# Kernel optimization log

Measured on AMD Instinct MI355X. Metric: run time of the kernel, lower is better.

The kernel has to match this reference:

```python
import jax, jax.numpy as jnp
import numpy as np

C_IN, C_INT = 256, 128


def setup_inputs() -> dict:
    key = jax.random.key(0)
    ks = jax.random.split(key, 7)
    B, H, W = 8, 64, 64
    s_in = 1.0 / np.sqrt(C_IN)
    return {
        "x": jax.random.normal(ks[0], (B, C_IN, H, W), dtype=jnp.float32),
        "w_theta": jax.random.uniform(ks[1], (C_INT, C_IN), jnp.float32, -s_in, s_in),
        "b_theta": jax.random.uniform(ks[2], (C_INT,), jnp.float32, -s_in, s_in),
        "w_phi": jax.random.uniform(ks[3], (C_INT, C_IN), jnp.float32, -s_in, s_in),
        "b_phi": jax.random.uniform(ks[4], (C_INT,), jnp.float32, -s_in, s_in),
        "w_g": jax.random.uniform(ks[5], (C_INT, C_IN), jnp.float32, -s_in, s_in),
        "b_g": jax.random.uniform(ks[6], (C_INT,), jnp.float32, -s_in, s_in),
    }


def reference(x, w_theta, b_theta, w_phi, b_phi, w_g, b_g):
    B, C, H, W = x.shape
    # flatten spatial: [B, N, C], 1x1 conv == per-position linear
    xf = x.reshape(B, C, H * W).transpose(0, 2, 1)  # [B, N, C_in]
    theta = jnp.einsum('bnc,dc->bnd', xf, w_theta) + b_theta  # [B, N, C_int]
    phi = jnp.einsum('bnc,dc->bnd', xf, w_phi) + b_phi        # [B, N, C_int]
    g = jnp.einsum('bnc,dc->bnd', xf, w_g) + b_g              # [B, N, C_int]
    f = jnp.einsum('bnd,bmd->bnm', theta, phi)  # [B, N, N] unscaled scores
    f_div_C = jax.nn.softmax(f, axis=-1)
    y = jnp.einsum('bnm,bmd->bnd', f_div_C, g)  # [B, N, C_int]
    # back to [B, C_int, H, W]
    return y.transpose(0, 2, 1).reshape(B, C_INT, H, W)
```

## Files before the change

### kernel.cpp

```cpp
#include <hip/hip_runtime.h>

typedef __attribute__((ext_vector_type(8))) short bf8;
typedef __attribute__((ext_vector_type(4))) float f4;
typedef unsigned short u16;

constexpr int B_ = 8, CIN = 256, CINT = 128, NN = 4096;
constexpr float L2E = 1.44269504088896f;

__device__ __forceinline__ u16 f2bf(float f) {
  unsigned int u = __builtin_bit_cast(unsigned int, f);
  u += 0x7FFFu + ((u >> 16) & 1u);
  return (u16)(u >> 16);
}

__device__ __forceinline__ void glds16(const void* g, void* l) {
  __builtin_amdgcn_global_load_lds(
      (const __attribute__((address_space(1))) unsigned int*)g,
      (__attribute__((address_space(3))) unsigned int*)l, 16, 0, 0);
}

__global__ __launch_bounds__(256) void prep_kernel(
    const float* __restrict__ wth, const float* __restrict__ wph,
    const float* __restrict__ wg, u16* __restrict__ wbf)
{
  int i = blockIdx.x * 256 + threadIdx.x;
  const float* src = (i < 32768) ? wth : (i < 65536) ? wph : wg;
  wbf[i] = f2bf(src[i & 32767]);
}

__global__ __launch_bounds__(256) void proj_kernel(
    const float* __restrict__ x, const u16* __restrict__ wbf,
    const float* __restrict__ bth, const float* __restrict__ bph,
    const float* __restrict__ bg,
    u16* __restrict__ theta, u16* __restrict__ phiT, u16* __restrict__ gTt)
{
  const int b = blockIdx.y, n0 = blockIdx.x * 64;
  const int tid = threadIdx.x, w = tid >> 6, l = tid & 63;
  const int lr = l & 15, lg = l >> 4;
  __shared__ __align__(16) u16 sx[64 * 256];

  const float* xb = x + (size_t)b * CIN * NN + n0;
  #pragma unroll
  for (int pass = 0; pass < 8; ++pass) {
    const int cb = w * 8 + pass * 32;
    u16 tmp[8];
    #pragma unroll
    for (int i = 0; i < 8; ++i) tmp[i] = f2bf(xb[(size_t)(cb + i) * NN + l]);
    uint4 v;
    v.x = (unsigned)tmp[0] | ((unsigned)tmp[1] << 16);
    v.y = (unsigned)tmp[2] | ((unsigned)tmp[3] << 16);
    v.z = (unsigned)tmp[4] | ((unsigned)tmp[5] << 16);
    v.w = (unsigned)tmp[6] | ((unsigned)tmp[7] << 16);
    *(uint4*)&sx[l * 256 + (((w + pass * 4) ^ (l & 7)) << 3)] = v;
  }
  __syncthreads();

  #pragma unroll
  for (int dti = 0; dti < 6; ++dti) {
    const int dt = w * 6 + dti;
    const int mat = dt >> 3, d0 = (dt & 7) * 16;
    const float* Bv = (mat == 0) ? bth : (mat == 1) ? bph : bg;
    const u16* wrow = wbf + mat * 32768 + (size_t)(d0 + lr) * 256 + lg * 8;
    bf8 wf[8];
    #pragma unroll
    for (int ks = 0; ks < 8; ++ks) wf[ks] = *(const bf8*)(wrow + ks * 32);

    #pragma unroll
    for (int mt = 0; mt < 4; ++mt) {
      f4 acc = {0.f, 0.f, 0.f, 0.f};
      const int row = mt * 16 + lr;
      #pragma unroll
      for (int ks = 0; ks < 8; ++ks) {
        bf8 bx = *(const bf8*)&sx[row * 256 + (((ks * 4 + lg) ^ (lr & 7)) << 3)];
        acc = __builtin_amdgcn_mfma_f32_16x16x32_bf16(wf[ks], bx, acc, 0, 0, 0);
      }
      const int m = n0 + mt * 16 + lr;
      const int dlo = d0 + lg * 4;
      if (mat == 0) {
        ushort4 h4;
        h4.x = f2bf(acc[0] + Bv[dlo + 0]);
        h4.y = f2bf(acc[1] + Bv[dlo + 1]);
        h4.z = f2bf(acc[2] + Bv[dlo + 2]);
        h4.w = f2bf(acc[3] + Bv[dlo + 3]);
        *(ushort4*)&theta[((size_t)b * NN + m) * CINT + dlo] = h4;
      } else if (mat == 1) {
        const int kt = m >> 5, r32 = m & 31;
        ushort4 h4;
        h4.x = f2bf((acc[0] + Bv[dlo + 0]) * L2E);
        h4.y = f2bf((acc[1] + Bv[dlo + 1]) * L2E);
        h4.z = f2bf((acc[2] + Bv[dlo + 2]) * L2E);
        h4.w = f2bf((acc[3] + Bv[dlo + 3]) * L2E);
        *(ushort4*)&phiT[((size_t)(b * 128 + kt)) * 4096 + r32 * 128 +
                         ((((dlo >> 3) ^ (r32 & 7))) << 3) + (dlo & 7)] = h4;
      } else {
        const int kt = m >> 5, kk = m & 31;
        #pragma unroll
        for (int r = 0; r < 4; ++r) {
          const int d = dlo + r;
          gTt[((size_t)(b * 128 + kt)) * 4096 + d * 32 +
              (((kk >> 3) ^ (d & 3)) << 3) + (kk & 7)] = f2bf(acc[r] + Bv[d]);
        }
      }
    }
  }
}

__global__ __launch_bounds__(512, 2) void attn_kernel(
    const u16* __restrict__ theta, const u16* __restrict__ phiT,
    const u16* __restrict__ gTt, float* __restrict__ out)
{
  const int b  = blockIdx.y;
  const int t_ = threadIdx.x;
  const int w  = t_ >> 6;
  const int l  = t_ & 63;
  const int lr = l & 15, lg = l >> 4;
  const int h  = w >> 2, wq = w & 3;
  const int qw = blockIdx.x * 128 + wq * 32;

  __shared__ __align__(16) char smem[106496];
  u16* sphi_base = (u16*)smem;
  u16* sg_base   = (u16*)(smem + 49152);
  u16* sPw       = (u16*)(smem + 98304 + w * 1024);

  const u16* th = theta + (size_t)b * NN * CINT;
  bf8 qf[2][4];
  #pragma unroll
  for (int qt = 0; qt < 2; ++qt)
    #pragma unroll
    for (int ds = 0; ds < 4; ++ds)
      qf[qt][ds] = *(const bf8*)(th + (size_t)(qw + qt * 16 + lr) * CINT + ds * 32 + lg * 8);

  f4 y[2][8];
  #pragma unroll
  for (int qt = 0; qt < 2; ++qt)
    #pragma unroll
    for (int dt = 0; dt < 8; ++dt) y[qt][dt] = (f4){0.f, 0.f, 0.f, 0.f};
  float rs[2] = {0.f, 0.f};

  const char* psrc = (const char*)(phiT + (size_t)(b * 128 + h * 64) * 4096);
  const char* gsrc = (const char*)(gTt + (size_t)(b * 128 + h * 64) * 4096);

  #define STAGE(BUF, T)                                                  \
    {                                                                    \
      const char* sp = psrc + (size_t)(T) * 8192 + wq * 2048 + l * 16;   \
      const char* sq = gsrc + (size_t)(T) * 8192 + wq * 2048 + l * 16;   \
      char* lp = (char*)(sphi_base + (h * 3 + (BUF)) * 4096) + wq * 2048;\
      char* lq = (char*)(sg_base + (h * 3 + (BUF)) * 4096) + wq * 2048;  \
      glds16(sp, lp); glds16(sp + 1024, lp + 1024);                      \
      glds16(sq, lq); glds16(sq + 1024, lq + 1024);                      \
    }

  constexpr int NT = 64;
  STAGE(0, 0);
  STAGE(1, 1);

  int bc = 0, bs = 2;
  for (int t = 0; t < NT; ++t) {
    if (t == NT - 1) asm volatile("s_waitcnt vmcnt(0)" ::: "memory");
    else             asm volatile("s_waitcnt vmcnt(4)" ::: "memory");
    __builtin_amdgcn_s_barrier();
    __builtin_amdgcn_sched_barrier(0);

    if (t < NT - 2) STAGE(bs, t + 2);

    const u16* PH = sphi_base + (h * 3 + bc) * 4096;
    const u16* GG = sg_base + (h * 3 + bc) * 4096;

    f4 s[2][2];
    s[0][0] = (f4){0.f,0.f,0.f,0.f}; s[0][1] = (f4){0.f,0.f,0.f,0.f};
    s[1][0] = (f4){0.f,0.f,0.f,0.f}; s[1][1] = (f4){0.f,0.f,0.f,0.f};
    __builtin_amdgcn_s_setprio(1);
    #pragma unroll
    for (int st = 0; st < 2; ++st) {
      const u16* base = PH + (st * 16 + lr) * 128;
      #pragma unroll
      for (int ds = 0; ds < 4; ++ds) {
        bf8 af = *(const bf8*)(base + (((ds * 4 + lg) ^ (lr & 7)) << 3));
        s[0][st] = __builtin_amdgcn_mfma_f32_16x16x32_bf16(af, qf[0][ds], s[0][st], 0, 0, 0);
        s[1][st] = __builtin_amdgcn_mfma_f32_16x16x32_bf16(af, qf[1][ds], s[1][st], 0, 0, 0);
      }
    }
    __builtin_amdgcn_s_setprio(0);

    bf8 gfr[8];
    #pragma unroll
    for (int dt = 0; dt < 8; ++dt)
      gfr[dt] = *(const bf8*)(GG + (dt * 16 + lr) * 32 + ((lg ^ (lr & 3)) << 3));

    #pragma unroll
    for (int qt = 0; qt < 2; ++qt) {
      float p0 = __builtin_amdgcn_exp2f(s[qt][0][0]);
      float p1 = __builtin_amdgcn_exp2f(s[qt][0][1]);
      float p2 = __builtin_amdgcn_exp2f(s[qt][0][2]);
      float p3 = __builtin_amdgcn_exp2f(s[qt][0][3]);
      float p4 = __builtin_amdgcn_exp2f(s[qt][1][0]);
      float p5 = __builtin_amdgcn_exp2f(s[qt][1][1]);
      float p6 = __builtin_amdgcn_exp2f(s[qt][1][2]);
      float p7 = __builtin_amdgcn_exp2f(s[qt][1][3]);
      rs[qt] += ((p0 + p1) + (p2 + p3)) + ((p4 + p5) + (p6 + p7));
      ushort4 pk;
      pk.x = f2bf(p0); pk.y = f2bf(p1); pk.z = f2bf(p2); pk.w = f2bf(p3);
      *(ushort4*)&sPw[lr * 32 + (((lg >> 1) ^ (lr & 3)) << 3) + ((lg & 1) << 2)] = pk;
      pk.x = f2bf(p4); pk.y = f2bf(p5); pk.z = f2bf(p6); pk.w = f2bf(p7);
      *(ushort4*)&sPw[lr * 32 + (((2 + (lg >> 1)) ^ (lr & 3)) << 3) + ((lg & 1) << 2)] = pk;

      bf8 paf = *(const bf8*)&sPw[lr * 32 + ((lg ^ (lr & 3)) << 3)];
      __builtin_amdgcn_s_setprio(1);
      #pragma unroll
      for (int dt = 0; dt < 8; ++dt)
        y[qt][dt] = __builtin_amdgcn_mfma_f32_16x16x32_bf16(paf, gfr[dt], y[qt][dt], 0, 0, 0);
      __builtin_amdgcn_s_setprio(0);
    }

    bc = (bc == 2) ? 0 : bc + 1;
    bs = (bs == 2) ? 0 : bs + 1;
  }

  #pragma unroll
  for (int qt = 0; qt < 2; ++qt) {
    rs[qt] += __shfl_xor(rs[qt], 16);
    rs[qt] += __shfl_xor(rs[qt], 32);
  }
  __syncthreads();
  float* ycomb  = (float*)smem;
  float* rscomb = (float*)(smem + 65536);
  if (h == 1) {
    #pragma unroll
    for (int qt = 0; qt < 2; ++qt) {
      #pragma unroll
      for (int dt = 0; dt < 8; ++dt)
        *(f4*)&ycomb[wq * 4096 + (qt * 8 + dt) * 256 + l * 4] = y[qt][dt];
      rscomb[wq * 128 + qt * 64 + l] = rs[qt];
    }
  }
  __syncthreads();
  if (h == 0) {
    #pragma unroll
    for (int qt = 0; qt < 2; ++qt) {
      #pragma unroll
      for (int dt = 0; dt < 8; ++dt)
        y[qt][dt] += *(const f4*)&ycomb[wq * 4096 + (qt * 8 + dt) * 256 + l * 4];
      rs[qt] += rscomb[wq * 128 + qt * 64 + l];
    }
    float* ob = out + (size_t)b * CINT * NN;
    #pragma unroll
    for (int qt = 0; qt < 2; ++qt) {
      f4 rsi;
      #pragma unroll
      for (int r = 0; r < 4; ++r)
        rsi[r] = 1.0f / __shfl(rs[qt], lg * 4 + r, 64);
      #pragma unroll
      for (int dt = 0; dt < 8; ++dt) {
        f4 v = y[qt][dt] * rsi;
        *(float4*)&ob[(size_t)(dt * 16 + lr) * NN + qw + qt * 16 + lg * 4] = *(float4*)&v;
      }
    }
  }
}

extern "C" void kernel_launch(void* const* d_in, const int* in_sizes, int n_in,
                              void* d_out, int out_size, void* d_ws, size_t ws_size,
                              hipStream_t stream) {
  const float* x   = (const float*)d_in[0];
  const float* wth = (const float*)d_in[1];
  const float* bth = (const float*)d_in[2];
  const float* wph = (const float*)d_in[3];
  const float* bph = (const float*)d_in[4];
  const float* wg  = (const float*)d_in[5];
  const float* bg  = (const float*)d_in[6];
  float* out = (float*)d_out;

  u16* theta = (u16*)d_ws;
  u16* phiT  = theta + (size_t)B_ * NN * CINT;
  u16* gTt   = phiT  + (size_t)B_ * NN * CINT;
  u16* wbf   = gTt   + (size_t)B_ * NN * CINT;

  hipLaunchKernelGGL(prep_kernel, dim3(384), dim3(256), 0, stream, wth, wph, wg, wbf);
  hipLaunchKernelGGL(proj_kernel, dim3(64, 8), dim3(256), 0, stream,
                     x, wbf, bth, bph, bg, theta, phiT, gTt);
  hipLaunchKernelGGL(attn_kernel, dim3(32, 8), dim3(512), 0, stream,
                     theta, phiT, gTt, out);
}
```

Baseline: 118.1 us.

## Transpose P in registers via permlane swaps and double-buffer phi/g tiles

```diff
diff --git a/kernel.cpp b/kernel.cpp
--- a/kernel.cpp
+++ b/kernel.cpp
@@ -17,6 +17,12 @@
   __builtin_amdgcn_global_load_lds(
       (const __attribute__((address_space(1))) unsigned int*)g,
       (__attribute__((address_space(3))) unsigned int*)l, 16, 0, 0);
+}
+
+__device__ __forceinline__ int cvtpk(float lo, float hi) {
+  int r;
+  asm("v_cvt_pk_bf16_f32 %0, %1, %2" : "=v"(r) : "v"(lo), "v"(hi));
+  return r;
 }
 
 __global__ __launch_bounds__(256) void prep_kernel(
@@ -97,8 +103,10 @@
         #pragma unroll
         for (int r = 0; r < 4; ++r) {
           const int d = dlo + r;
-          gTt[((size_t)(b * 128 + kt)) * 4096 + d * 32 +
-              (((kk >> 3) ^ (d & 3)) << 3) + (kk & 7)] = f2bf(acc[r] + Bv[d]);
+          const int grow = d >> 1;
+          const int chunk = (((d & 1) * 4 + (kk >> 3)) ^ (grow & 7));
+          gTt[((size_t)(b * 128 + kt)) * 4096 + grow * 64 + chunk * 8 + (kk & 7)]
+              = f2bf(acc[r] + Bv[d]);
         }
       }
     }
@@ -117,10 +125,9 @@
   const int h  = w >> 2, wq = w & 3;
   const int qw = blockIdx.x * 128 + wq * 32;
 
-  __shared__ __align__(16) char smem[106496];
-  u16* sphi_base = (u16*)smem;
-  u16* sg_base   = (u16*)(smem + 49152);
-  u16* sPw       = (u16*)(smem + 98304 + w * 1024);
+  __shared__ __align__(16) char smem[67584];
+  u16* sphi_b = (u16*)smem;
+  u16* sg_b   = (u16*)(smem + 32768);
 
   const u16* th = theta + (size_t)b * NN * CINT;
   bf8 qf[2][4];
@@ -137,34 +144,32 @@
     for (int dt = 0; dt < 8; ++dt) y[qt][dt] = (f4){0.f, 0.f, 0.f, 0.f};
   float rs[2] = {0.f, 0.f};
 
-  const char* psrc = (const char*)(phiT + (size_t)(b * 128 + h * 64) * 4096);
-  const char* gsrc = (const char*)(gTt + (size_t)(b * 128 + h * 64) * 4096);
-
-  #define STAGE(BUF, T)                                                  \
-    {                                                                    \
-      const char* sp = psrc + (size_t)(T) * 8192 + wq * 2048 + l * 16;   \
-      const char* sq = gsrc + (size_t)(T) * 8192 + wq * 2048 + l * 16;   \
-      char* lp = (char*)(sphi_base + (h * 3 + (BUF)) * 4096) + wq * 2048;\
-      char* lq = (char*)(sg_base + (h * 3 + (BUF)) * 4096) + wq * 2048;  \
-      glds16(sp, lp); glds16(sp + 1024, lp + 1024);                      \
-      glds16(sq, lq); glds16(sq + 1024, lq + 1024);                      \
-    }
-
-  constexpr int NT = 64;
+  const char* psrc = (const char*)(phiT + (size_t)(b * 128 + h * 64) * 4096) +
+                     wq * 2048 + l * 16;
+  const char* gsrc = (const char*)(gTt + (size_t)(b * 128 + h * 64) * 4096) +
+                     wq * 2048 + l * 16;
+
+  #define STAGE(BUF, T)                                                    \
+    {                                                                      \
+      const char* sp = psrc + (size_t)(T) * 8192;                          \
+      const char* sq = gsrc + (size_t)(T) * 8192;                          \
+      char* lp = (char*)(sphi_b + (h * 2 + (BUF)) * 4096) + wq * 2048;     \
+      char* lq = (char*)(sg_b + (h * 2 + (BUF)) * 4096) + wq * 2048;       \
+      glds16(sp, lp); glds16(sp + 1024, lp + 1024);                        \
+      glds16(sq, lq); glds16(sq + 1024, lq + 1024);                        \
+    }
+
   STAGE(0, 0);
-  STAGE(1, 1);
-
-  int bc = 0, bs = 2;
-  for (int t = 0; t < NT; ++t) {
-    if (t == NT - 1) asm volatile("s_waitcnt vmcnt(0)" ::: "memory");
-    else             asm volatile("s_waitcnt vmcnt(4)" ::: "memory");
-    __builtin_amdgcn_s_barrier();
-    __builtin_amdgcn_sched_barrier(0);
-
-    if (t < NT - 2) STAGE(bs, t + 2);
-
-    const u16* PH = sphi_base + (h * 3 + bc) * 4096;
-    const u16* GG = sg_base + (h * 3 + bc) * 4096;
+  asm volatile("s_waitcnt vmcnt(0)" ::: "memory");
+  __builtin_amdgcn_s_barrier();
+  __builtin_amdgcn_sched_barrier(0);
+
+  int cur = 0;
+  for (int t = 0; t < 64; ++t) {
+    if (t < 63) STAGE(cur ^ 1, t + 1);
+
+    const u16* PH = sphi_b + (h * 2 + cur) * 4096;
+    const u16* GG = sg_b + (h * 2 + cur) * 4096;
 
     f4 s[2][2];
     s[0][0] = (f4){0.f,0.f,0.f,0.f}; s[0][1] = (f4){0.f,0.f,0.f,0.f};
@@ -184,8 +189,11 @@
 
     bf8 gfr[8];
     #pragma unroll
-    for (int dt = 0; dt < 8; ++dt)
-      gfr[dt] = *(const bf8*)(GG + (dt * 16 + lr) * 32 + ((lg ^ (lr & 3)) << 3));
+    for (int dt = 0; dt < 8; ++dt) {
+      const int grow = dt * 8 + (lr >> 1);
+      const int chunk = (((lr & 1) * 4 + lg) ^ (grow & 7));
+      gfr[dt] = *(const bf8*)(GG + grow * 64 + chunk * 8);
+    }
 
     #pragma unroll
     for (int qt = 0; qt < 2; ++qt) {
@@ -198,13 +206,16 @@
       float p6 = __builtin_amdgcn_exp2f(s[qt][1][2]);
       float p7 = __builtin_amdgcn_exp2f(s[qt][1][3]);
       rs[qt] += ((p0 + p1) + (p2 + p3)) + ((p4 + p5) + (p6 + p7));
-      ushort4 pk;
-      pk.x = f2bf(p0); pk.y = f2bf(p1); pk.z = f2bf(p2); pk.w = f2bf(p3);
-      *(ushort4*)&sPw[lr * 32 + (((lg >> 1) ^ (lr & 3)) << 3) + ((lg & 1) << 2)] = pk;
-      pk.x = f2bf(p4); pk.y = f2bf(p5); pk.z = f2bf(p6); pk.w = f2bf(p7);
-      *(ushort4*)&sPw[lr * 32 + (((2 + (lg >> 1)) ^ (lr & 3)) << 3) + ((lg & 1) << 2)] = pk;
-
-      bf8 paf = *(const bf8*)&sPw[lr * 32 + ((lg ^ (lr & 3)) << 3)];
+
+      int w0 = cvtpk(p0, p1), w1 = cvtpk(p2, p3);
+      int w2 = cvtpk(p4, p5), w3 = cvtpk(p6, p7);
+      asm volatile("v_permlane32_swap_b32 %0, %1" : "+v"(w0), "+v"(w2));
+      asm volatile("v_permlane16_swap_b32 %0, %1" : "+v"(w0), "+v"(w2));
+      asm volatile("v_permlane32_swap_b32 %0, %1" : "+v"(w1), "+v"(w3));
+      asm volatile("v_permlane16_swap_b32 %0, %1" : "+v"(w1), "+v"(w3));
+      int pai[4] = {w0, w1, w2, w3};
+      bf8 paf = __builtin_bit_cast(bf8, *(int4*)pai);
+
       __builtin_amdgcn_s_setprio(1);
       #pragma unroll
       for (int dt = 0; dt < 8; ++dt)
@@ -212,8 +223,10 @@
       __builtin_amdgcn_s_setprio(0);
     }
 
-    bc = (bc == 2) ? 0 : bc + 1;
-    bs = (bs == 2) ? 0 : bs + 1;
+    if (t < 63) asm volatile("s_waitcnt vmcnt(0)" ::: "memory");
+    __builtin_amdgcn_s_barrier();
+    __builtin_amdgcn_sched_barrier(0);
+    cur ^= 1;
   }
 
   #pragma unroll
```

Result: faster. 104.7 us (-11.4%).
